# Kernel optimization log

Measured on AMD Instinct MI355X. Metric: run time of the kernel, lower is better.

Reference implementation:

```python
import jax, jax.numpy as jnp
import numpy as np

P, B, D, H, O = 512, 8, 256, 75, 128  # passage_len, batch, input_size, attn hidden, GRU hidden


def setup_inputs() -> dict:
    key = jax.random.key(0)
    ks = jax.random.split(key, 10)

    def w(k, shape, fan_in):
        return jax.random.normal(k, shape, jnp.float32) * (1.0 / np.sqrt(fan_in))

    return {
        "v": jax.random.normal(ks[0], (P, B, D), jnp.float32),
        "Wvp1": w(ks[1], (H, D), D),          # nn.Linear(input_size, hidden, bias=False)
        "Wvp2": w(ks[2], (H, D), D),
        "vw": w(ks[3], (H,), H),               # nn.Linear(hidden, 1, bias=False)
        "Wg": w(ks[4], (2 * D, 2 * D), 2 * D),  # Gate linear, no bias
        "w_ih_f": w(ks[5], (3 * O, 2 * D), 2 * D),
        "w_hh_f": w(ks[6], (3 * O, O), O),
        "b_ih_f": jnp.zeros((3 * O,), jnp.float32),
        "b_hh_f": jnp.zeros((3 * O,), jnp.float32),
        "w_ih_b": w(ks[7], (3 * O, 2 * D), 2 * D),
        "w_hh_b": w(ks[8], (3 * O, O), O),
        "b_ih_b": jnp.zeros((3 * O,), jnp.float32),
        "b_hh_b": jnp.zeros((3 * O,), jnp.float32),
    }


def _gru(x, w_ih, w_hh, b_ih, b_hh):
    # x: (T, B, in) -> hidden states (T, B, O); PyTorch GRU gate order (r, z, n)
    hdim = w_hh.shape[1]
    xp = x @ w_ih.T + b_ih  # precompute input projections: (T, B, 3O)

    def step(h, xp_t):
        gh = h @ w_hh.T + b_hh
        i_r, i_z, i_n = jnp.split(xp_t, 3, axis=-1)
        h_r, h_z, h_n = jnp.split(gh, 3, axis=-1)
        r = jax.nn.sigmoid(i_r + h_r)
        z = jax.nn.sigmoid(i_z + h_z)
        n = jnp.tanh(i_n + r * h_n)
        h_new = (1.0 - z) * n + z * h
        return h_new, h_new

    h0 = jnp.zeros((x.shape[1], hdim), x.dtype)
    _, hs = jax.lax.scan(step, h0, xp)
    return hs


def reference(v, Wvp1, Wvp2, vw, Wg,
              w_ih_f, w_hh_f, b_ih_f, b_hh_f,
              w_ih_b, w_hh_b, b_ih_b, b_hh_b):
    # dropout is inference no-op (and in the torch code its result is discarded anyway)
    Wv1 = v @ Wvp1.T  # (P, B, H) -- broadcast over key axis (dim 1 after expand)
    Wv2 = v @ Wvp2.T  # (P, B, H) -- broadcast over query axis
    # s[i, j, b, h] = tanh(Wv2[i] + Wv1[j]); softmax over i (keys)
    s = jnp.tanh(Wv2[:, None] + Wv1[None, :])          # (P, P, B, H)
    scores = jnp.einsum('ijbh,h->ijb', s, vw)          # (P, P, B)
    a = jax.nn.softmax(scores, axis=0)
    c = jnp.einsum('ijb,ibd->jbd', a, v)               # attended context (P, B, D)
    g = jnp.concatenate([v, c], axis=2)                # (P, B, 2D)
    g = jax.nn.sigmoid(g @ Wg.T) * g                   # Gate
    hf = _gru(g, w_ih_f, w_hh_f, b_ih_f, b_hh_f)
    hb = _gru(g[::-1], w_ih_b, w_hh_b, b_ih_b, b_hh_b)[::-1]
    return jnp.concatenate([hf, hb], axis=2)           # (P, B, 2O)
```

## Files before the change

kernel.cpp:

```cpp
#include <hip/hip_runtime.h>

#define TP 512
#define TB 8
#define TD 256
#define TH 75
#define THP 80
#define TO 128

typedef _Float16 half_t;
typedef _Float16 half2v __attribute__((ext_vector_type(2)));
typedef _Float16 half4v __attribute__((ext_vector_type(4)));
typedef _Float16 half8v __attribute__((ext_vector_type(8)));
typedef float    float4v __attribute__((ext_vector_type(4)));

__device__ __forceinline__ float fast_rcp(float x) { return __builtin_amdgcn_rcpf(x); }
__device__ __forceinline__ float fast_tanh(float x) {
    return 1.0f - 2.0f * fast_rcp(1.0f + __expf(2.0f * x));
}
__device__ __forceinline__ float fast_sigmoid(float x) {
    return fast_rcp(1.0f + __expf(-x));
}
__device__ __forceinline__ float fdot2h(half2v a, half2v b, float c) {
#if __has_builtin(__builtin_amdgcn_fdot2)
    return __builtin_amdgcn_fdot2(a, b, c, false);
#else
    return c + (float)a[0] * (float)b[0] + (float)a[1] * (float)b[1];
#endif
}
#define EXT2(v, j) __builtin_shufflevector((v), (v), 2*(j), 2*(j)+1)
__device__ __forceinline__ void dot3_h8(half8v wr, half8v wz, half8v wn, half8v h,
                                        float& ar, float& az, float& an) {
    half2v h0 = EXT2(h, 0), h1 = EXT2(h, 1), h2 = EXT2(h, 2), h3 = EXT2(h, 3);
    ar = fdot2h(EXT2(wr, 0), h0, ar);
    az = fdot2h(EXT2(wz, 0), h0, az);
    an = fdot2h(EXT2(wn, 0), h0, an);
    ar = fdot2h(EXT2(wr, 1), h1, ar);
    az = fdot2h(EXT2(wz, 1), h1, az);
    an = fdot2h(EXT2(wn, 1), h1, an);
    ar = fdot2h(EXT2(wr, 2), h2, ar);
    az = fdot2h(EXT2(wz, 2), h2, az);
    an = fdot2h(EXT2(wn, 2), h2, an);
    ar = fdot2h(EXT2(wr, 3), h3, ar);
    az = fdot2h(EXT2(wz, 3), h3, az);
    an = fdot2h(EXT2(wn, 3), h3, an);
}
__device__ __forceinline__ float pair_sum_dpp(float v) {
    int i1 = __builtin_amdgcn_update_dpp(0, __builtin_bit_cast(int, v), 0xB1, 0xF, 0xF, true);
    return v + __builtin_bit_cast(float, i1);
}

__global__ __launch_bounds__(256) void prep_kernel(
    const float* __restrict__ v,
    const float* __restrict__ Wvp1, const float* __restrict__ Wvp2,
    const float* __restrict__ Wg,   const float* __restrict__ wihf,
    const float* __restrict__ wihb, const float* __restrict__ bihf,
    const float* __restrict__ bihb, const float* __restrict__ whhf,
    const float* __restrict__ whhb,
    float* __restrict__ bihC,
    half_t* __restrict__ v16, half_t* __restrict__ g16,
    half_t* __restrict__ Wg16B, half_t* __restrict__ Wih16B,
    half_t* __restrict__ whh16, half_t* __restrict__ WT16B)
{
    int idx = blockIdx.x * 256 + threadIdx.x;
    if (idx < 1048576) {
        half_t val = (half_t)v[idx];
        v16[idx] = val;
        int row = idx >> 8, d = idx & 255;
        g16[row * 512 + d] = val;
        return;
    }
    idx -= 1048576;
    if (idx < 768) { bihC[idx] = (idx < 384) ? bihf[idx] : bihb[idx - 384]; return; }
    idx -= 768;
    if (idx < 262144) {
        int j = idx & 7, lane = (idx >> 3) & 63, kt = (idx >> 9) & 15, nt = idx >> 13;
        int o = nt * 16 + (lane & 15);
        int k = kt * 32 + ((lane >> 4) << 3) + j;
        Wg16B[idx] = (half_t)Wg[o * 512 + k];
        return;
    }
    idx -= 262144;
    if (idx < 393216) {
        int j = idx & 7, lane = (idx >> 3) & 63, kt = (idx >> 9) & 15, nt = idx >> 13;
        int o = nt * 16 + (lane & 15);
        int k = kt * 32 + ((lane >> 4) << 3) + j;
        Wih16B[idx] = (half_t)((o < 384) ? wihf[o * 512 + k] : wihb[(o - 384) * 512 + k]);
        return;
    }
    idx -= 393216;
    if (idx < 98304) {
        int d = idx / 49152, i = idx - d * 49152;
        whh16[idx] = (half_t)(d ? whhb[i] : whhf[i]);
        return;
    }
    idx -= 98304;
    if (idx < 40960) {
        int j = idx & 7, lane = (idx >> 3) & 63, kt = (idx >> 9) & 7, nt = idx >> 12;
        int o = nt * 16 + (lane & 15);
        int k = kt * 32 + ((lane >> 4) << 3) + j;
        float vv = 0.0f;
        if (o < 75)       vv = Wvp1[o * 256 + k];
        else if (o < 150) vv = Wvp2[(o - 75) * 256 + k];
        WT16B[idx] = (half_t)vv;
    }
}

__global__ __launch_bounds__(256) void vtrans_kernel(
    const float* __restrict__ v, half_t* __restrict__ vT16)
{
    __shared__ half_t lt[64 * 66];
    int t = threadIdx.x;
    int b  = blockIdx.x >> 5;
    int pt = (blockIdx.x >> 2) & 7;
    int dt = blockIdx.x & 3;

    {
        int pl = t >> 2, dseg = (t & 3) * 16;
        const float4* src = (const float4*)(v + (((pt * 64 + pl) * 8 + b) << 8) + dt * 64 + dseg);
        float4 f0 = src[0], f1 = src[1], f2 = src[2], f3 = src[3];
        half_t hv[16] = {
            (half_t)f0.x,(half_t)f0.y,(half_t)f0.z,(half_t)f0.w,
            (half_t)f1.x,(half_t)f1.y,(half_t)f1.z,(half_t)f1.w,
            (half_t)f2.x,(half_t)f2.y,(half_t)f2.z,(half_t)f2.w,
            (half_t)f3.x,(half_t)f3.y,(half_t)f3.z,(half_t)f3.w };
#pragma unroll
        for (int u = 0; u < 16; ++u) lt[(dseg + u) * 66 + pl] = hv[u];
    }
    __syncthreads();
    {
        int dl = t >> 2, pseg = (t & 3) * 16;
        half8v h0 = *(const half8v*)(lt + dl * 66 + pseg);
        half8v h1 = *(const half8v*)(lt + dl * 66 + pseg + 8);
        half8v* dst = (half8v*)(vT16 + ((b * 256 + dt * 64 + dl) << 9) + pt * 64 + pseg);
        dst[0] = h0; dst[1] = h1;
    }
}

__global__ __launch_bounds__(256) void wv12_kernel(
    const half_t* __restrict__ v16, const half_t* __restrict__ WT16B,
    float* __restrict__ Wv1, float* __restrict__ Wv2T)
{
    int tid = threadIdx.x;
    int lane = tid & 63, w = tid >> 6;
    int l15 = lane & 15, quad = lane >> 4;
    int r0 = blockIdx.x * 64 + w * 16;

    float4v acc[10];
#pragma unroll
    for (int nt = 0; nt < 10; ++nt) acc[nt] = (float4v){0.f, 0.f, 0.f, 0.f};

#pragma unroll
    for (int kt = 0; kt < 8; ++kt) {
        half8v a = *(const half8v*)(v16 + (r0 + l15) * 256 + kt * 32 + quad * 8);
#pragma unroll
        for (int nt = 0; nt < 10; ++nt) {
            half8v b = *(const half8v*)(WT16B + ((nt * 8 + kt) * 64 + lane) * 8);
            acc[nt] = __builtin_amdgcn_mfma_f32_16x16x32_f16(a, b, acc[nt], 0, 0, 0);
        }
    }
#pragma unroll
    for (int nt = 0; nt < 10; ++nt) {
        int col = nt * 16 + l15;
#pragma unroll
        for (int r = 0; r < 4; ++r) {
            int row = r0 + quad * 4 + r;
            int p = row >> 3, b = row & 7;
            int ob = (b * TP + p) * THP;
            float val2 = 2.0f * acc[nt][r];
            if (col < 75)       Wv1[ob + col] = val2;
            else if (col < 80)  { Wv1[ob + col] = 0.0f;
                                  Wv2T[(b * THP + col - 75) * TP + p] = val2; }
            else if (col < 150) Wv2T[(b * THP + col - 75) * TP + p] = val2;
            else if (col < 155) Wv2T[(b * THP + col - 75) * TP + p] = 0.0f;
        }
    }
}

__global__ __launch_bounds__(256) void score_kernel(
    const float* __restrict__ Wv1, const float* __restrict__ Wv2T,
    const float* __restrict__ vw, half_t* __restrict__ a16)
{
    int tid = threadIdx.x;
    int b  = blockIdx.x >> 7;
    int j0 = (blockIdx.x & 127) * 4;
    __shared__ float wv1j[4 * THP];
    __shared__ float vws[THP];
    __shared__ float sc[4 * TP];

    if (tid < THP) vws[tid] = (tid < TH) ? vw[tid] : 0.0f;
    for (int e = tid; e < 4 * THP; e += 256) {
        int jj = e / THP, k = e - jj * THP;
        wv1j[e] = Wv1[(b * TP + j0 + jj) * THP + k];
    }
    __syncthreads();

    float Csum = 0.0f;
    {
        const float4* c4 = (const float4*)vws;
        for (int kk = 0; kk < 20; ++kk) { float4 c = c4[kk]; Csum += c.x + c.y + c.z + c.w; }
    }

    int i0 = tid, i1 = tid + 256;
    float acc0[4] = {0.f,0.f,0.f,0.f}, acc1[4] = {0.f,0.f,0.f,0.f};
    const float* wvt = Wv2T + b * THP * TP;
#pragma unroll
    for (int kt = 0; kt < 5; ++kt) {
        float r0v[16], r1v[16];
#pragma unroll
        for (int u = 0; u < 16; ++u) {
            const float* colp = wvt + (kt * 16 + u) * TP;
            r0v[u] = colp[i0];
            r1v[u] = colp[i1];
        }
        const float* cp = vws + kt * 16;
#pragma unroll
        for (int jj = 0; jj < 4; ++jj) {
            const float* w1 = wv1j + jj * THP + kt * 16;
            float s0 = 0.f, s1 = 0.f;
#pragma unroll
            for (int u = 0; u < 16; ++u) {
                float cu = cp[u], wu = w1[u];
                s0 += cu * fast_rcp(1.0f + __expf(r0v[u] + wu));
                s1 += cu * fast_rcp(1.0f + __expf(r1v[u] + wu));
            }
            acc0[jj] += s0; acc1[jj] += s1;
        }
    }
#pragma unroll
    for (int jj = 0; jj < 4; ++jj) {
        sc[jj * TP + i0] = Csum - 2.0f * acc0[jj];
        sc[jj * TP + i1] = Csum - 2.0f * acc1[jj];
    }
    __syncthreads();

    {
        int jj = tid >> 6, l = tid & 63;
        float m = -1e30f;
#pragma unroll
        for (int q = 0; q < 8; ++q) m = fmaxf(m, sc[jj * TP + l + q * 64]);
#pragma unroll
        for (int s = 32; s > 0; s >>= 1) m = fmaxf(m, __shfl_xor(m, s));
        float e[8];
        float sum = 0.0f;
#pragma unroll
        for (int q = 0; q < 8; ++q) { e[q] = __expf(sc[jj * TP + l + q * 64] - m); sum += e[q]; }
#pragma unroll
        for (int s = 32; s > 0; s >>= 1) sum += __shfl_xor(sum, s);
        float inv = fast_rcp(sum);
        half_t* arow = a16 + (b * TP + j0 + jj) * TP;
#pragma unroll
        for (int q = 0; q < 8; ++q) arow[l + q * 64] = (half_t)(e[q] * inv);
    }
}

__global__ __launch_bounds__(256) void context_kernel(
    const half_t* __restrict__ a16, const half_t* __restrict__ vT16,
    half_t* __restrict__ g16)
{
    int tid = threadIdx.x;
    int lane = tid & 63, w = tid >> 6;
    int l15 = lane & 15, quad = lane >> 4;
    int b  = blockIdx.x >> 5;
    int mt = blockIdx.x & 31;

    const half_t* arow = a16 + (b * TP + mt * 16 + l15) * TP;
    const half_t* vbase = vT16 + ((b * 256) << 9);

    float4v acc[4];
#pragma unroll
    for (int nti = 0; nti < 4; ++nti) acc[nti] = (float4v){0.f, 0.f, 0.f, 0.f};

#pragma unroll 4
    for (int kt = 0; kt < 16; ++kt) {
        half8v a = *(const half8v*)(arow + kt * 32 + quad * 8);
#pragma unroll
        for (int nti = 0; nti < 4; ++nti) {
            int d = (w * 4 + nti) * 16 + l15;
            half8v bb = *(const half8v*)(vbase + (d << 9) + kt * 32 + quad * 8);
            acc[nti] = __builtin_amdgcn_mfma_f32_16x16x32_f16(a, bb, acc[nti], 0, 0, 0);
        }
    }
#pragma unroll
    for (int nti = 0; nti < 4; ++nti) {
        int d = (w * 4 + nti) * 16 + l15;
#pragma unroll
        for (int r = 0; r < 4; ++r) {
            int j = mt * 16 + quad * 4 + r;
            g16[(j * TB + b) * 512 + 256 + d] = (half_t)acc[nti][r];
        }
    }
}

__global__ __launch_bounds__(256, 1) void gatexp_kernel(
    const half_t* __restrict__ g16, const half_t* __restrict__ Wg16B,
    const half_t* __restrict__ Wih16B, const float* __restrict__ bihC,
    float* __restrict__ xpf, float* __restrict__ xpb)
{
    __shared__ half_t gA[32 * 520];
    int tid = threadIdx.x;
    int r0 = blockIdx.x * 32;
    int lane = tid & 63, w = tid >> 6;
    int l15 = lane & 15, quad = lane >> 4;

    for (int e = tid; e < 2048; e += 256) {
        int row = e >> 6, c8 = e & 63;
        *(half8v*)(gA + row * 520 + c8 * 8) =
            *(const half8v*)(g16 + (r0 + row) * 512 + c8 * 8);
    }
    __syncthreads();

    float4v acc[2][8];
#pragma unroll
    for (int mi = 0; mi < 2; ++mi)
#pragma unroll
        for (int nti = 0; nti < 8; ++nti) acc[mi][nti] = (float4v){0.f, 0.f, 0.f, 0.f};

    for (int kt = 0; kt < 16; ++kt) {
        half8v a0 = *(const half8v*)(gA + l15 * 520 + kt * 32 + quad * 8);
        half8v a1 = *(const half8v*)(gA + (16 + l15) * 520 + kt * 32 + quad * 8);
#pragma unroll
        for (int nti = 0; nti < 8; ++nti) {
            half8v bb = *(const half8v*)(Wg16B + (((w * 8 + nti) * 16 + kt) * 64 + lane) * 8);
            acc[0][nti] = __builtin_amdgcn_mfma_f32_16x16x32_f16(a0, bb, acc[0][nti], 0, 0, 0);
            acc[1][nti] = __builtin_amdgcn_mfma_f32_16x16x32_f16(a1, bb, acc[1][nti], 0, 0, 0);
        }
    }
#pragma unroll
    for (int mi = 0; mi < 2; ++mi)
#pragma unroll
        for (int nti = 0; nti < 8; ++nti) {
            int colg = (w * 8 + nti) * 16 + l15;
#pragma unroll
            for (int r = 0; r < 4; ++r) {
                float gv = (float)gA[(mi * 16 + quad * 4 + r) * 520 + colg];
                acc[mi][nti][r] = fast_sigmoid(acc[mi][nti][r]) * gv;
            }
        }
    __syncthreads();
#pragma unroll
    for (int mi = 0; mi < 2; ++mi)
#pragma unroll
        for (int nti = 0; nti < 8; ++nti) {
            int colg = (w * 8 + nti) * 16 + l15;
#pragma unroll
            for (int r = 0; r < 4; ++r)
                gA[(mi * 16 + quad * 4 + r) * 520 + colg] = (half_t)acc[mi][nti][r];
        }
    __syncthreads();

    float4v c2[2][12];
#pragma unroll
    for (int mi = 0; mi < 2; ++mi)
#pragma unroll
        for (int nt2 = 0; nt2 < 12; ++nt2) {
            float bv = bihC[(w * 12 + nt2) * 16 + l15];
            c2[mi][nt2] = (float4v){bv, bv, bv, bv};
        }

    for (int kt = 0; kt < 16; ++kt) {
        half8v a0 = *(const half8v*)(gA + l15 * 520 + kt * 32 + quad * 8);
        half8v a1 = *(const half8v*)(gA + (16 + l15) * 520 + kt * 32 + quad * 8);
#pragma unroll
        for (int nt2 = 0; nt2 < 12; ++nt2) {
            half8v bb = *(const half8v*)(Wih16B + (((w * 12 + nt2) * 16 + kt) * 64 + lane) * 8);
            c2[0][nt2] = __builtin_amdgcn_mfma_f32_16x16x32_f16(a0, bb, c2[0][nt2], 0, 0, 0);
            c2[1][nt2] = __builtin_amdgcn_mfma_f32_16x16x32_f16(a1, bb, c2[1][nt2], 0, 0, 0);
        }
    }
#pragma unroll
    for (int mi = 0; mi < 2; ++mi)
#pragma unroll
        for (int nt2 = 0; nt2 < 12; ++nt2) {
            int col = (w * 12 + nt2) * 16 + l15;
            float* dst = (col < 384) ? (xpf + col) : (xpb + col - 384);
#pragma unroll
            for (int r = 0; r < 4; ++r)
                dst[(r0 + mi * 16 + quad * 4 + r) * 384] = c2[mi][nt2][r];
        }
}

__global__ __launch_bounds__(256) void gru_kernel(
    const float* __restrict__ xpf, const float* __restrict__ xpb,
    const half_t* __restrict__ whh16,
    const float* __restrict__ bhhf, const float* __restrict__ bhhb,
    float* __restrict__ out)
{
    int tid = threadIdx.x;
    int dir = blockIdx.x >> 3;
    int b   = blockIdx.x & 7;
    const float* xp  = dir ? xpb  : xpf;
    const float* bhh = dir ? bhhb : bhhf;
    const half_t* wbase = whh16 + dir * 3 * TO * TO;

    __shared__ __align__(16) half_t hb[2][TO];

    int o = tid >> 1, hf = tid & 1;

    half8v wr[8], wz[8], wn[8];
    {
        const half8v* pr = (const half8v*)(wbase + (o)          * TO + hf * 64);
        const half8v* pz = (const half8v*)(wbase + (TO + o)     * TO + hf * 64);
        const half8v* pn = (const half8v*)(wbase + (2 * TO + o) * TO + hf * 64);
#pragma unroll
        for (int kk = 0; kk < 8; ++kk) { wr[kk] = pr[kk]; wz[kk] = pz[kk]; wn[kk] = pn[kk]; }
    }

    float br = 0.f, bz = 0.f, bn = 0.f, h = 0.f;
    if (hf == 0) {
        br = bhh[o]; bz = bhh[TO + o]; bn = bhh[2 * TO + o];
    }
    if (tid < TO) hb[0][tid] = (half_t)0.0f;
    __syncthreads();

    float xrv[8], xzv[8], xnv[8], hist[8];

    for (int S = 0; S < TP; S += 8) {
        if (hf == 0) {
#pragma unroll
            for (int u = 0; u < 8; ++u) {
                int s = S + u;
                int tn = dir ? (TP - 1 - s) : s;
                const float* xpt = xp + (tn * TB + b) * 384;
                xrv[u] = xpt[o]; xzv[u] = xpt[TO + o]; xnv[u] = xpt[2 * TO + o];
            }
        }
#pragma unroll
        for (int u = 0; u < 8; ++u) {
            int s = S + u;
            int cur = s & 1;
            const half8v* h8 = (const half8v*)(&hb[cur][hf * 64]);
            half8v hv0 = h8[0], hv1 = h8[1], hv2 = h8[2], hv3 = h8[3];
            half8v hv4 = h8[4], hv5 = h8[5], hv6 = h8[6], hv7 = h8[7];

            float ar = 0.f, az = 0.f, an = 0.f;
            dot3_h8(wr[0], wz[0], wn[0], hv0, ar, az, an);
            dot3_h8(wr[1], wz[1], wn[1], hv1, ar, az, an);
            dot3_h8(wr[2], wz[2], wn[2], hv2, ar, az, an);
            dot3_h8(wr[3], wz[3], wn[3], hv3, ar, az, an);
            dot3_h8(wr[4], wz[4], wn[4], hv4, ar, az, an);
            dot3_h8(wr[5], wz[5], wn[5], hv5, ar, az, an);
            dot3_h8(wr[6], wz[6], wn[6], hv6, ar, az, an);
            dot3_h8(wr[7], wz[7], wn[7], hv7, ar, az, an);

            ar = pair_sum_dpp(ar);
            az = pair_sum_dpp(az);
            an = pair_sum_dpp(an);
            if (hf == 0) {
                float r = fast_sigmoid(xrv[u] + ar + br);
                float z = fast_sigmoid(xzv[u] + az + bz);
                float n = fast_tanh(xnv[u] + r * (an + bn));
                h = (1.0f - z) * n + z * h;
                hb[cur ^ 1][o] = (half_t)h;
                hist[u] = h;
            }
            __syncthreads();
        }
        if (hf == 0) {
#pragma unroll
            for (int u = 0; u < 8; ++u) {
                int s = S + u;
                int t = dir ? (TP - 1 - s) : s;
                out[(t * TB + b) * 256 + dir * TO + o] = hist[u];
            }
        }
    }
}

extern "C" void kernel_launch(void* const* d_in, const int* in_sizes, int n_in,
                              void* d_out, int out_size, void* d_ws, size_t ws_size,
                              hipStream_t stream) {
    const float* v    = (const float*)d_in[0];
    const float* Wvp1 = (const float*)d_in[1];
    const float* Wvp2 = (const float*)d_in[2];
    const float* vw   = (const float*)d_in[3];
    const float* Wg   = (const float*)d_in[4];
    const float* wihf = (const float*)d_in[5];
    const float* whhf = (const float*)d_in[6];
    const float* bihf = (const float*)d_in[7];
    const float* bhhf = (const float*)d_in[8];
    const float* wihb = (const float*)d_in[9];
    const float* whhb = (const float*)d_in[10];
    const float* bihb = (const float*)d_in[11];
    const float* bhhb = (const float*)d_in[12];

    float* ws   = (float*)d_ws;
    float* bihC = ws;
    float* Wv1  = bihC + 768;
    float* Wv2T = Wv1 + 327680;
    float* xpf  = Wv2T + 327680;
    float* xpb  = xpf + 1572864;
    half_t* g16    = (half_t*)(xpb + 1572864);
    half_t* Wg16B  = g16 + 2097152;
    half_t* Wih16B = Wg16B + 262144;
    half_t* whh16  = Wih16B + 393216;
    half_t* v16    = whh16 + 98304;
    half_t* WT16B  = v16 + 1048576;
    half_t* vT16   = WT16B + 40960;
    half_t* a16    = vT16 + 1048576;
    float* out  = (float*)d_out;

    prep_kernel<<<7203, 256, 0, stream>>>(v, Wvp1, Wvp2, Wg, wihf, wihb, bihf, bihb,
                                          whhf, whhb, bihC, v16, g16,
                                          Wg16B, Wih16B, whh16, WT16B);
    vtrans_kernel<<<256, 256, 0, stream>>>(v, vT16);
    wv12_kernel<<<64, 256, 0, stream>>>(v16, WT16B, Wv1, Wv2T);
    score_kernel<<<1024, 256, 0, stream>>>(Wv1, Wv2T, vw, a16);
    context_kernel<<<256, 256, 0, stream>>>(a16, vT16, g16);
    gatexp_kernel<<<128, 256, 0, stream>>>(g16, Wg16B, Wih16B, bihC, xpf, xpb);
    gru_kernel<<<16, 256, 0, stream>>>(xpf, xpb, whh16, bhhf, bhhb, out);
}
```

Baseline: 440.7 us.

## Prefetch next GRU input projections and lighten per-step barrier

The GRU recurrence kernel now loads the next 8 timesteps of input projections into registers while the current 8 steps are computed, hiding global-load latency behind the serial recurrence. The per-step __syncthreads is replaced by an explicit LDS waitcnt plus s_barrier, which avoids waiting on outstanding global loads (vmcnt) so the prefetch stays in flight. Launch bounds pin one block per CU and an empty asm keeps the weight vectors in VGPRs. This costs 24 extra registers per thread and relies on the memory ordering of the hand-written barrier being correct.

```diff
diff --git a/kernel.cpp b/kernel.cpp
--- a/kernel.cpp
+++ b/kernel.cpp
@@ -379,7 +379,7 @@
         }
 }
 
-__global__ __launch_bounds__(256) void gru_kernel(
+__global__ __launch_bounds__(256, 1) void gru_kernel(
     const float* __restrict__ xpf, const float* __restrict__ xpb,
     const half_t* __restrict__ whh16,
     const float* __restrict__ bhhf, const float* __restrict__ bhhb,
@@ -404,6 +404,10 @@
 #pragma unroll
         for (int kk = 0; kk < 8; ++kk) { wr[kk] = pr[kk]; wz[kk] = pz[kk]; wn[kk] = pn[kk]; }
     }
+#pragma unroll
+    for (int kk = 0; kk < 8; ++kk) {
+        asm volatile("" : "+v"(wr[kk]), "+v"(wz[kk]), "+v"(wn[kk]));
+    }
 
     float br = 0.f, bz = 0.f, bn = 0.f, h = 0.f;
     if (hf == 0) {
@@ -412,16 +416,31 @@
     if (tid < TO) hb[0][tid] = (half_t)0.0f;
     __syncthreads();
 
-    float xrv[8], xzv[8], xnv[8], hist[8];
+    float xrv[8], xzv[8], xnv[8];
+    float nxr[8], nxz[8], nxn[8];
+    float hist[8];
+
+    if (hf == 0) {
+#pragma unroll
+        for (int u = 0; u < 8; ++u) {
+            int tn = dir ? (TP - 1 - u) : u;
+            const float* xpt = xp + (tn * TB + b) * 384;
+            nxr[u] = xpt[o]; nxz[u] = xpt[TO + o]; nxn[u] = xpt[2 * TO + o];
+        }
+    }
 
     for (int S = 0; S < TP; S += 8) {
         if (hf == 0) {
 #pragma unroll
-            for (int u = 0; u < 8; ++u) {
-                int s = S + u;
-                int tn = dir ? (TP - 1 - s) : s;
-                const float* xpt = xp + (tn * TB + b) * 384;
-                xrv[u] = xpt[o]; xzv[u] = xpt[TO + o]; xnv[u] = xpt[2 * TO + o];
+            for (int u = 0; u < 8; ++u) { xrv[u] = nxr[u]; xzv[u] = nxz[u]; xnv[u] = nxn[u]; }
+            if (S + 8 < TP) {
+#pragma unroll
+                for (int u = 0; u < 8; ++u) {
+                    int s = S + 8 + u;
+                    int tn = dir ? (TP - 1 - s) : s;
+                    const float* xpt = xp + (tn * TB + b) * 384;
+                    nxr[u] = xpt[o]; nxz[u] = xpt[TO + o]; nxn[u] = xpt[2 * TO + o];
+                }
             }
         }
 #pragma unroll
@@ -453,7 +472,9 @@
                 hb[cur ^ 1][o] = (half_t)h;
                 hist[u] = h;
             }
-            __syncthreads();
+            asm volatile("s_waitcnt lgkmcnt(0)" ::: "memory");
+            __builtin_amdgcn_s_barrier();
+            __builtin_amdgcn_sched_barrier(0);
         }
         if (hf == 0) {
 #pragma unroll
```

Result: slower. 456.8 us (+3.7%).

## Use MFMA for GRU recurrent matvec with pre-scaled exp2 gate activations

Applied to the files above, without the earlier changes.

Replaces the per-thread fdot2 recurrent matvec in the GRU step with 16x16x32 MFMA instructions. The recurrent weights are prepacked into MFMA B-fragment layout and held in AGPRs, and the hidden state sits in padded, swizzled LDS with only row 0 meaningful. Weights and biases are prescaled by -log2e or 2*log2e so sigmoid and tanh reduce to exp2 plus rcp. The next step's input projections are prefetched one step ahead and outputs are written every step. This aims to shorten the serial per-step latency, but only 16 of 64 lanes per wave do the activation math and the MFMA computes 15 wasted rows.

```diff
diff --git a/kernel.cpp b/kernel.cpp
--- a/kernel.cpp
+++ b/kernel.cpp
@@ -7,6 +7,9 @@
 #define THP 80
 #define TO 128
 
+#define SCRZ (-1.4426950408889634f)
+#define SCN  ( 2.8853900817779268f)
+
 typedef _Float16 half_t;
 typedef _Float16 half2v __attribute__((ext_vector_type(2)));
 typedef _Float16 half4v __attribute__((ext_vector_type(4)));
@@ -14,39 +17,15 @@
 typedef float    float4v __attribute__((ext_vector_type(4)));
 
 __device__ __forceinline__ float fast_rcp(float x) { return __builtin_amdgcn_rcpf(x); }
-__device__ __forceinline__ float fast_tanh(float x) {
-    return 1.0f - 2.0f * fast_rcp(1.0f + __expf(2.0f * x));
+__device__ __forceinline__ float ex2(float x) {
+#if __has_builtin(__builtin_amdgcn_exp2f)
+    return __builtin_amdgcn_exp2f(x);
+#else
+    float r; asm("v_exp_f32 %0, %1" : "=v"(r) : "v"(x)); return r;
+#endif
 }
 __device__ __forceinline__ float fast_sigmoid(float x) {
     return fast_rcp(1.0f + __expf(-x));
-}
-__device__ __forceinline__ float fdot2h(half2v a, half2v b, float c) {
-#if __has_builtin(__builtin_amdgcn_fdot2)
-    return __builtin_amdgcn_fdot2(a, b, c, false);
-#else
-    return c + (float)a[0] * (float)b[0] + (float)a[1] * (float)b[1];
-#endif
-}
-#define EXT2(v, j) __builtin_shufflevector((v), (v), 2*(j), 2*(j)+1)
-__device__ __forceinline__ void dot3_h8(half8v wr, half8v wz, half8v wn, half8v h,
-                                        float& ar, float& az, float& an) {
-    half2v h0 = EXT2(h, 0), h1 = EXT2(h, 1), h2 = EXT2(h, 2), h3 = EXT2(h, 3);
-    ar = fdot2h(EXT2(wr, 0), h0, ar);
-    az = fdot2h(EXT2(wz, 0), h0, az);
-    an = fdot2h(EXT2(wn, 0), h0, an);
-    ar = fdot2h(EXT2(wr, 1), h1, ar);
-    az = fdot2h(EXT2(wz, 1), h1, az);
-    an = fdot2h(EXT2(wn, 1), h1, an);
-    ar = fdot2h(EXT2(wr, 2), h2, ar);
-    az = fdot2h(EXT2(wz, 2), h2, az);
-    an = fdot2h(EXT2(wn, 2), h2, an);
-    ar = fdot2h(EXT2(wr, 3), h3, ar);
-    az = fdot2h(EXT2(wz, 3), h3, az);
-    an = fdot2h(EXT2(wn, 3), h3, an);
-}
-__device__ __forceinline__ float pair_sum_dpp(float v) {
-    int i1 = __builtin_amdgcn_update_dpp(0, __builtin_bit_cast(int, v), 0xB1, 0xF, 0xF, true);
-    return v + __builtin_bit_cast(float, i1);
 }
 
 __global__ __launch_bounds__(256) void prep_kernel(
@@ -59,7 +38,7 @@
     float* __restrict__ bihC,
     half_t* __restrict__ v16, half_t* __restrict__ g16,
     half_t* __restrict__ Wg16B, half_t* __restrict__ Wih16B,
-    half_t* __restrict__ whh16, half_t* __restrict__ WT16B)
+    half_t* __restrict__ whhB, half_t* __restrict__ WT16B)
 {
     int idx = blockIdx.x * 256 + threadIdx.x;
     if (idx < 1048576) {
@@ -70,7 +49,12 @@
         return;
     }
     idx -= 1048576;
-    if (idx < 768) { bihC[idx] = (idx < 384) ? bihf[idx] : bihb[idx - 384]; return; }
+    if (idx < 768) {
+        int c = (idx < 384) ? idx : idx - 384;
+        float sc = ((c >> 7) == 2) ? SCN : SCRZ;
+        bihC[idx] = sc * ((idx < 384) ? bihf[idx] : bihb[idx - 384]);
+        return;
+    }
     idx -= 768;
     if (idx < 262144) {
         int j = idx & 7, lane = (idx >> 3) & 63, kt = (idx >> 9) & 15, nt = idx >> 13;
@@ -84,13 +68,21 @@
         int j = idx & 7, lane = (idx >> 3) & 63, kt = (idx >> 9) & 15, nt = idx >> 13;
         int o = nt * 16 + (lane & 15);
         int k = kt * 32 + ((lane >> 4) << 3) + j;
-        Wih16B[idx] = (half_t)((o < 384) ? wihf[o * 512 + k] : wihb[(o - 384) * 512 + k]);
+        float wv_ = (o < 384) ? wihf[o * 512 + k] : wihb[(o - 384) * 512 + k];
+        int og = ((o < 384) ? o : o - 384) >> 7;
+        float sc = (og == 2) ? SCN : SCRZ;
+        Wih16B[idx] = (half_t)(wv_ * sc);
         return;
     }
     idx -= 393216;
     if (idx < 98304) {
         int d = idx / 49152, i = idx - d * 49152;
-        whh16[idx] = (half_t)(d ? whhb[i] : whhf[i]);
+        int j = i & 7, lane = (i >> 3) & 63, kt = (i >> 9) & 3, nt = i >> 11;
+        int n = nt * 16 + (lane & 15);
+        int k = kt * 32 + ((lane >> 4) << 3) + j;
+        float sc = (nt >= 16) ? SCN : SCRZ;
+        const float* src = d ? whhb : whhf;
+        whhB[idx] = (half_t)(sc * src[n * 128 + k]);
         return;
     }
     idx -= 98304;
@@ -379,9 +371,9 @@
         }
 }
 
-__global__ __launch_bounds__(256) void gru_kernel(
+__global__ __launch_bounds__(256, 1) void gru_kernel(
     const float* __restrict__ xpf, const float* __restrict__ xpb,
-    const half_t* __restrict__ whh16,
+    const half_t* __restrict__ whhB,
     const float* __restrict__ bhhf, const float* __restrict__ bhhb,
     float* __restrict__ out)
 {
@@ -390,79 +382,103 @@
     int b   = blockIdx.x & 7;
     const float* xp  = dir ? xpb  : xpf;
     const float* bhh = dir ? bhhb : bhhf;
-    const half_t* wbase = whh16 + dir * 3 * TO * TO;
-
-    __shared__ __align__(16) half_t hb[2][TO];
-
-    int o = tid >> 1, hf = tid & 1;
-
-    half8v wr[8], wz[8], wn[8];
-    {
-        const half8v* pr = (const half8v*)(wbase + (o)          * TO + hf * 64);
-        const half8v* pz = (const half8v*)(wbase + (TO + o)     * TO + hf * 64);
-        const half8v* pn = (const half8v*)(wbase + (2 * TO + o) * TO + hf * 64);
-#pragma unroll
-        for (int kk = 0; kk < 8; ++kk) { wr[kk] = pr[kk]; wz[kk] = pz[kk]; wn[kk] = pn[kk]; }
-    }
-
-    float br = 0.f, bz = 0.f, bn = 0.f, h = 0.f;
-    if (hf == 0) {
-        br = bhh[o]; bz = bhh[TO + o]; bn = bhh[2 * TO + o];
-    }
-    if (tid < TO) hb[0][tid] = (half_t)0.0f;
-    __syncthreads();
-
-    float xrv[8], xzv[8], xnv[8], hist[8];
-
-    for (int S = 0; S < TP; S += 8) {
-        if (hf == 0) {
-#pragma unroll
-            for (int u = 0; u < 8; ++u) {
-                int s = S + u;
-                int tn = dir ? (TP - 1 - s) : s;
-                const float* xpt = xp + (tn * TB + b) * 384;
-                xrv[u] = xpt[o]; xzv[u] = xpt[TO + o]; xnv[u] = xpt[2 * TO + o];
+    const half_t* wb = whhB + dir * 49152;
+
+    __shared__ __align__(16) half_t H[2][16][128];
+
+    int lane = tid & 63, w = tid >> 6;
+    int l15 = lane & 15, quad = lane >> 4;
+
+    for (int e = tid; e < 4096; e += 256) (&H[0][0][0])[e] = (half_t)0.0f;
+
+    half8v B_[2][3][4];
+#pragma unroll
+    for (int g = 0; g < 2; ++g)
+#pragma unroll
+        for (int gt = 0; gt < 3; ++gt)
+#pragma unroll
+            for (int kt = 0; kt < 4; ++kt) {
+                int nt = gt * 8 + (2 * w + g);
+                B_[g][gt][kt] = *(const half8v*)(wb + ((nt * 4 + kt) * 64 + lane) * 8);
             }
-        }
-#pragma unroll
-        for (int u = 0; u < 8; ++u) {
-            int s = S + u;
-            int cur = s & 1;
-            const half8v* h8 = (const half8v*)(&hb[cur][hf * 64]);
-            half8v hv0 = h8[0], hv1 = h8[1], hv2 = h8[2], hv3 = h8[3];
-            half8v hv4 = h8[4], hv5 = h8[5], hv6 = h8[6], hv7 = h8[7];
-
-            float ar = 0.f, az = 0.f, an = 0.f;
-            dot3_h8(wr[0], wz[0], wn[0], hv0, ar, az, an);
-            dot3_h8(wr[1], wz[1], wn[1], hv1, ar, az, an);
-            dot3_h8(wr[2], wz[2], wn[2], hv2, ar, az, an);
-            dot3_h8(wr[3], wz[3], wn[3], hv3, ar, az, an);
-            dot3_h8(wr[4], wz[4], wn[4], hv4, ar, az, an);
-            dot3_h8(wr[5], wz[5], wn[5], hv5, ar, az, an);
-            dot3_h8(wr[6], wz[6], wn[6], hv6, ar, az, an);
-            dot3_h8(wr[7], wz[7], wn[7], hv7, ar, az, an);
-
-            ar = pair_sum_dpp(ar);
-            az = pair_sum_dpp(az);
-            an = pair_sum_dpp(an);
-            if (hf == 0) {
-                float r = fast_sigmoid(xrv[u] + ar + br);
-                float z = fast_sigmoid(xzv[u] + az + bz);
-                float n = fast_tanh(xnv[u] + r * (an + bn));
-                h = (1.0f - z) * n + z * h;
-                hb[cur ^ 1][o] = (half_t)h;
-                hist[u] = h;
+#pragma unroll
+    for (int g = 0; g < 2; ++g)
+#pragma unroll
+        for (int gt = 0; gt < 3; ++gt)
+#pragma unroll
+            for (int kt = 0; kt < 4; ++kt) {
+                float4v t = __builtin_bit_cast(float4v, B_[g][gt][kt]);
+                asm volatile("" : "+a"(t));
+                B_[g][gt][kt] = __builtin_bit_cast(half8v, t);
             }
-            __syncthreads();
-        }
-        if (hf == 0) {
-#pragma unroll
-            for (int u = 0; u < 8; ++u) {
-                int s = S + u;
-                int t = dir ? (TP - 1 - s) : s;
-                out[(t * TB + b) * 256 + dir * TO + o] = hist[u];
+
+    int ro[4];
+#pragma unroll
+    for (int kt = 0; kt < 4; ++kt)
+        ro[kt] = (l15 * 256 + kt * 64 + quad * 16) ^ ((l15 & 7) << 4);
+
+    bool act = (lane < 16);
+    int o0 = (2 * w) * 16 + l15, o1 = o0 + 16;
+    float br0=0,bz0=0,bn0=0,br1=0,bz1=0,bn1=0, h0=0.f, h1=0.f;
+    float pr0=0,pz0=0,pn0=0,pr1=0,pz1=0,pn1=0;
+    if (act) {
+        br0 = SCRZ * bhh[o0]; bz0 = SCRZ * bhh[TO + o0]; bn0 = SCN * bhh[2*TO + o0];
+        br1 = SCRZ * bhh[o1]; bz1 = SCRZ * bhh[TO + o1]; bn1 = SCN * bhh[2*TO + o1];
+        int tn = dir ? (TP - 1) : 0;
+        const float* xq = xp + (tn * TB + b) * 384;
+        pr0 = xq[o0]; pz0 = xq[TO + o0]; pn0 = xq[2*TO + o0];
+        pr1 = xq[o1]; pz1 = xq[TO + o1]; pn1 = xq[2*TO + o1];
+    }
+    __syncthreads();
+
+    const char* Hc = (const char*)&H[0][0][0];
+    const float4v z4 = {0.f, 0.f, 0.f, 0.f};
+    int cur = 0;
+    for (int s = 0; s < TP; ++s) {
+        float xr0 = pr0, xz0 = pz0, xn0 = pn0;
+        float xr1 = pr1, xz1 = pz1, xn1 = pn1;
+        if (act && s + 1 < TP) {
+            int tn = dir ? (TP - 2 - s) : (s + 1);
+            const float* xq = xp + (tn * TB + b) * 384;
+            pr0 = xq[o0]; pz0 = xq[TO + o0]; pn0 = xq[2*TO + o0];
+            pr1 = xq[o1]; pz1 = xq[TO + o1]; pn1 = xq[2*TO + o1];
+        }
+
+        half8v A0 = *(const half8v*)(Hc + cur * 4096 + ro[0]);
+        half8v A1 = *(const half8v*)(Hc + cur * 4096 + ro[1]);
+        half8v A2 = *(const half8v*)(Hc + cur * 4096 + ro[2]);
+        half8v A3 = *(const half8v*)(Hc + cur * 4096 + ro[3]);
+
+        float4v acc[2][3];
+#pragma unroll
+        for (int g = 0; g < 2; ++g)
+#pragma unroll
+            for (int gt = 0; gt < 3; ++gt) {
+                float4v c = __builtin_amdgcn_mfma_f32_16x16x32_f16(A0, B_[g][gt][0], z4, 0, 0, 0);
+                c = __builtin_amdgcn_mfma_f32_16x16x32_f16(A1, B_[g][gt][1], c, 0, 0, 0);
+                c = __builtin_amdgcn_mfma_f32_16x16x32_f16(A2, B_[g][gt][2], c, 0, 0, 0);
+                acc[g][gt] = __builtin_amdgcn_mfma_f32_16x16x32_f16(A3, B_[g][gt][3], c, 0, 0, 0);
             }
-        }
+
+        if (act) {
+            float rr = fast_rcp(1.0f + ex2(acc[0][0][0] + xr0 + br0));
+            float zz = fast_rcp(1.0f + ex2(acc[0][1][0] + xz0 + bz0));
+            float nn = 1.0f - 2.0f * fast_rcp(1.0f + ex2(xn0 + rr * (acc[0][2][0] + bn0)));
+            h0 = nn + zz * (h0 - nn);
+            float rr1 = fast_rcp(1.0f + ex2(acc[1][0][0] + xr1 + br1));
+            float zz1 = fast_rcp(1.0f + ex2(acc[1][1][0] + xz1 + bz1));
+            float nn1 = 1.0f - 2.0f * fast_rcp(1.0f + ex2(xn1 + rr1 * (acc[1][2][0] + bn1)));
+            h1 = nn1 + zz1 * (h1 - nn1);
+            H[cur ^ 1][0][o0] = (half_t)h0;
+            H[cur ^ 1][0][o1] = (half_t)h1;
+        }
+        __syncthreads();
+        if (act) {
+            int tn = dir ? (TP - 1 - s) : s;
+            out[(tn * TB + b) * 256 + dir * TO + o0] = h0;
+            out[(tn * TB + b) * 256 + dir * TO + o1] = h1;
+        }
+        cur ^= 1;
     }
 }
 
@@ -492,8 +508,8 @@
     half_t* g16    = (half_t*)(xpb + 1572864);
     half_t* Wg16B  = g16 + 2097152;
     half_t* Wih16B = Wg16B + 262144;
-    half_t* whh16  = Wih16B + 393216;
-    half_t* v16    = whh16 + 98304;
+    half_t* whhB   = Wih16B + 393216;
+    half_t* v16    = whhB + 98304;
     half_t* WT16B  = v16 + 1048576;
     half_t* vT16   = WT16B + 40960;
     half_t* a16    = vT16 + 1048576;
@@ -501,11 +517,11 @@
 
     prep_kernel<<<7203, 256, 0, stream>>>(v, Wvp1, Wvp2, Wg, wihf, wihb, bihf, bihb,
                                           whhf, whhb, bihC, v16, g16,
-                                          Wg16B, Wih16B, whh16, WT16B);
+                                          Wg16B, Wih16B, whhB, WT16B);
     vtrans_kernel<<<256, 256, 0, stream>>>(v, vT16);
     wv12_kernel<<<64, 256, 0, stream>>>(v16, WT16B, Wv1, Wv2T);
     score_kernel<<<1024, 256, 0, stream>>>(Wv1, Wv2T, vw, a16);
     context_kernel<<<256, 256, 0, stream>>>(a16, vT16, g16);
     gatexp_kernel<<<128, 256, 0, stream>>>(g16, Wg16B, Wih16B, bihC, xpf, xpb);
-    gru_kernel<<<16, 256, 0, stream>>>(xpf, xpb, whh16, bhhf, bhhb, out);
-}
+    gru_kernel<<<16, 256, 0, stream>>>(xpf, xpb, whhB, bhhf, bhhb, out);
+}
```

Measured after the change: 505.5 us. 1.15x slower.
